# Performance work log

Measured on AMD Instinct MI355X. Metric: run time of the kernel, lower is better.

## Reference

```python
import jax, jax.numpy as jnp
import numpy as np

T, D, K = 8192, 1024, 1024
LMBDA = 5.0
BIG = jnp.float32(3.0e38)  # finite stand-in for +inf so (f - lmbda) stays finite


def setup_inputs() -> dict:
    key = jax.random.key(0)
    k1, k2 = jax.random.split(key)
    return {
        "features": jax.random.normal(k1, (T, D), dtype=jnp.float32),
        "codebook": jax.random.normal(k2, (K, D), dtype=jnp.float32),
    }


def _dpdp(features, codebook, lmbda):
    # squared euclidean distances, (T, K)
    d2 = (
        jnp.sum(features * features, axis=1, keepdims=True)
        - 2.0 * features @ codebook.T
        + jnp.sum(codebook * codebook, axis=1)
    )
    Tn = features.shape[0]
    Kn = codebook.shape[0]

    # Incremental O(T*K) form of the original O(T^2*K) recurrence:
    # f_t[k] = min_{s<=t-1} alpha[s] - lmbda*(t-1-s) + sum_{i=s..t-1} d2[i,k]
    #        = d2[t-1,k] + min(alpha[t-1], f_{t-1}[k] - lmbda)
    # alpha[t] = min_k f_t[k]; beta[t] = start index s of argmin; gamma[t] = argmin_k.
    def fwd_step(carry, inp):
        f, s, alpha = carry  # f:(K,), s:(K,) segment start per codeword, alpha: scalar
        d_t, t = inp
        ext = f - lmbda                      # extend existing segment
        take_new = alpha < ext               # start a new segment at t
        f_new = d_t + jnp.minimum(alpha, ext)
        s_new = jnp.where(take_new, t, s)
        k_star = jnp.argmin(f_new)
        alpha_new = f_new[k_star]
        return (f_new, s_new, alpha_new), (s_new[k_star], k_star.astype(jnp.int32))

    init = (jnp.full((Kn,), BIG, jnp.float32), jnp.zeros((Kn,), jnp.int32), jnp.float32(0.0))
    ts = jnp.arange(Tn, dtype=jnp.int32)
    _, (betas, gammas) = jax.lax.scan(fwd_step, init, (d2, ts))
    # betas[t-1]/gammas[t-1] correspond to alpha index t in the original code.

    # Backtrack: units[beta[cur]:cur] = gamma[cur]; cur = beta[cur].
    def bwd_step(cur, p):
        g = gammas[cur - 1]
        b = betas[cur - 1]
        cur_new = jnp.where(p == b, p, cur)
        return cur_new, g

    _, units = jax.lax.scan(bwd_step, jnp.int32(Tn), ts, reverse=True)
    return units


def reference(features, codebook):
    units = _dpdp(features, codebook, LMBDA)
    quantized = codebook[units]
    quantized_st = features - jax.lax.stop_gradient(features - quantized)
    return quantized_st, units
```

## Files before the change

### kernel.cpp

```cpp
#include <hip/hip_runtime.h>
#include <hip/hip_bf16.h>
#include <stdint.h>

#define T_N 8192
#define K_N 1024
#define D_N 1024
#define LMBDA 5.0f
#define BIGF 3.0e38f
#define CMAX 16
#define THR 26.0f
#define QNAN 0x7FC00000

__global__ __launch_bounds__(256) void k_norms(const float* __restrict__ F,
                                               const float* __restrict__ C,
                                               float* __restrict__ sf2,
                                               float* __restrict__ sc2) {
#pragma clang fp contract(off)
  int wave = threadIdx.x >> 6;
  int lane = threadIdx.x & 63;
  int row = blockIdx.x * 4 + wave;
  const float* src;
  float* dst;
  if (row < T_N) { src = F + (size_t)row * D_N; dst = sf2 + row; }
  else           { src = C + (size_t)(row - T_N) * D_N; dst = sc2 + (row - T_N); }
  int leaf = lane >> 3, j = lane & 7;
  const float* p = src + leaf * 128 + j;
  float x = p[0];
  float r = x * x;
#pragma unroll
  for (int i = 1; i < 16; ++i) {
    float y = p[8 * i];
    r = r + y * y;
  }
  r = r + __shfl_xor(r, 1, 64);
  r = r + __shfl_xor(r, 2, 64);
  r = r + __shfl_xor(r, 4, 64);
  r = r + __shfl_xor(r, 8, 64);
  r = r + __shfl_xor(r, 16, 64);
  r = r + __shfl_xor(r, 32, 64);
  if (lane == 0) *dst = r;
}

__global__ __launch_bounds__(256) void k_gemm(const float* __restrict__ F,
                                              const float* __restrict__ C,
                                              const float* __restrict__ sf2,
                                              const float* __restrict__ sc2,
                                              float* __restrict__ d2) {
  __shared__ float As[32][68];
  __shared__ float Bs[32][132];
  int t0 = (int)(blockIdx.x >> 3) * 64;
  int k0 = (int)(blockIdx.x & 7) * 128;
  int tid = threadIdx.x;
  int tx = tid & 15, ty = tid >> 4;
  float dot[4][8], acc[4][8];
#pragma unroll
  for (int i = 0; i < 4; ++i)
#pragma unroll
    for (int j = 0; j < 8; ++j) { dot[i][j] = 0.0f; acc[i][j] = 0.0f; }
  int ra = tid & 63, ca = (tid >> 6) * 8;
  int rb = tid & 127, cb = (tid >> 7) * 16;
  for (int d0 = 0; d0 < D_N; d0 += 32) {
    __syncthreads();
    {
      const float* fa = &F[(size_t)(t0 + ra) * D_N + d0 + ca];
      float4 a0 = *(const float4*)fa;
      float4 a1 = *(const float4*)(fa + 4);
      As[ca + 0][ra] = a0.x; As[ca + 1][ra] = a0.y; As[ca + 2][ra] = a0.z; As[ca + 3][ra] = a0.w;
      As[ca + 4][ra] = a1.x; As[ca + 5][ra] = a1.y; As[ca + 6][ra] = a1.z; As[ca + 7][ra] = a1.w;
      const float* fb = &C[(size_t)(k0 + rb) * D_N + d0 + cb];
      float4 b0 = *(const float4*)fb;
      float4 b1 = *(const float4*)(fb + 4);
      float4 b2 = *(const float4*)(fb + 8);
      float4 b3 = *(const float4*)(fb + 12);
      Bs[cb + 0][rb] = b0.x; Bs[cb + 1][rb] = b0.y; Bs[cb + 2][rb] = b0.z; Bs[cb + 3][rb] = b0.w;
      Bs[cb + 4][rb] = b1.x; Bs[cb + 5][rb] = b1.y; Bs[cb + 6][rb] = b1.z; Bs[cb + 7][rb] = b1.w;
      Bs[cb + 8][rb] = b2.x; Bs[cb + 9][rb] = b2.y; Bs[cb + 10][rb] = b2.z; Bs[cb + 11][rb] = b2.w;
      Bs[cb + 12][rb] = b3.x; Bs[cb + 13][rb] = b3.y; Bs[cb + 14][rb] = b3.z; Bs[cb + 15][rb] = b3.w;
    }
    __syncthreads();
#pragma unroll
    for (int d = 0; d < 32; ++d) {
      float4 a = *(const float4*)&As[d][ty * 4];
      float4 b0 = *(const float4*)&Bs[d][tx * 4];
      float4 b1 = *(const float4*)&Bs[d][64 + tx * 4];
      float av[4] = {a.x, a.y, a.z, a.w};
      float bv[8] = {b0.x, b0.y, b0.z, b0.w, b1.x, b1.y, b1.z, b1.w};
#pragma unroll
      for (int i = 0; i < 4; ++i)
#pragma unroll
        for (int j = 0; j < 8; ++j)
          acc[i][j] = fmaf(av[i], bv[j], acc[i][j]);
    }
    if (d0 == 352) {
#pragma unroll
      for (int i = 0; i < 4; ++i)
#pragma unroll
        for (int j = 0; j < 8; ++j) { dot[i][j] = acc[i][j]; acc[i][j] = 0.0f; }
    }
    if (d0 == 736) {
#pragma unroll
      for (int i = 0; i < 4; ++i)
#pragma unroll
        for (int j = 0; j < 8; ++j) { dot[i][j] = dot[i][j] + acc[i][j]; acc[i][j] = 0.0f; }
    }
  }
  {
#pragma clang fp contract(off)
#pragma unroll
    for (int i = 0; i < 4; ++i) {
      int t = t0 + ty * 4 + i;
      float sa = sf2[t];
      float o[8];
#pragma unroll
      for (int j = 0; j < 4; ++j) {
        float dsum = dot[i][j] + acc[i][j];
        float two = 2.0f * dsum;
        o[j] = (sa - two) + sc2[k0 + tx * 4 + j];
      }
#pragma unroll
      for (int j = 4; j < 8; ++j) {
        float dsum = dot[i][j] + acc[i][j];
        float two = 2.0f * dsum;
        o[j] = (sa - two) + sc2[k0 + 64 + tx * 4 + (j - 4)];
      }
      float4 o0; o0.x = o[0]; o0.y = o[1]; o0.z = o[2]; o0.w = o[3];
      float4 o1; o1.x = o[4]; o1.y = o[5]; o1.z = o[6]; o1.w = o[7];
      float* dp = &d2[(size_t)t * K_N + k0 + tx * 4];
      *(float4*)dp = o0;
      *(float4*)(dp + 64) = o1;
    }
  }
}

__global__ __launch_bounds__(256) void k_cand(const float* __restrict__ d2,
                                              int2* __restrict__ cand,
                                              float* __restrict__ dminOut) {
  int wave = threadIdx.x >> 6;
  int lane = threadIdx.x & 63;
  int row = blockIdx.x * 4 + wave;
  const float4* p = (const float4*)(d2 + (size_t)row * K_N + lane * 16);
  float4 v0 = p[0], v1 = p[1], v2 = p[2], v3 = p[3];
  float m = fminf(fminf(fminf(v0.x, v0.y), fminf(v0.z, v0.w)),
                  fminf(fminf(v1.x, v1.y), fminf(v1.z, v1.w)));
  float n = fminf(fminf(fminf(v2.x, v2.y), fminf(v2.z, v2.w)),
                  fminf(fminf(v3.x, v3.y), fminf(v3.z, v3.w)));
  m = fminf(m, n);
  m = fminf(m, __shfl_xor(m, 1, 64));
  m = fminf(m, __shfl_xor(m, 2, 64));
  m = fminf(m, __shfl_xor(m, 4, 64));
  m = fminf(m, __shfl_xor(m, 8, 64));
  m = fminf(m, __shfl_xor(m, 16, 64));
  m = fminf(m, __shfl_xor(m, 32, 64));
  if (lane == 0) dminOut[row] = m;
  float thr = m + THR;
  unsigned flags = 0;
#define TESTC(J, VAL) if ((VAL) <= thr) flags |= (1u << (J));
  TESTC(0, v0.x) TESTC(1, v0.y) TESTC(2, v0.z) TESTC(3, v0.w)
  TESTC(4, v1.x) TESTC(5, v1.y) TESTC(6, v1.z) TESTC(7, v1.w)
  TESTC(8, v2.x) TESTC(9, v2.y) TESTC(10, v2.z) TESTC(11, v2.w)
  TESTC(12, v3.x) TESTC(13, v3.y) TESTC(14, v3.z) TESTC(15, v3.w)
#undef TESTC
  int c = __popc(flags);
  int pre = c;
#pragma unroll
  for (int off = 1; off <= 32; off <<= 1) {
    int t = __shfl_up(pre, off, 64);
    if (lane >= off) pre += t;
  }
  int idx = pre - c;
  int2* rowp = cand + (size_t)row * CMAX;
  int kb = lane * 16;
#define EMITC(J, VAL)                                                        \
  if (flags & (1u << (J))) {                                                 \
    if (idx < CMAX) rowp[idx] = make_int2(kb + (J), __float_as_int(VAL));    \
    ++idx;                                                                   \
  }
  EMITC(0, v0.x) EMITC(1, v0.y) EMITC(2, v0.z) EMITC(3, v0.w)
  EMITC(4, v1.x) EMITC(5, v1.y) EMITC(6, v1.z) EMITC(7, v1.w)
  EMITC(8, v2.x) EMITC(9, v2.y) EMITC(10, v2.z) EMITC(11, v2.w)
  EMITC(12, v3.x) EMITC(13, v3.y) EMITC(14, v3.z) EMITC(15, v3.w)
#undef EMITC
}

__global__ __launch_bounds__(256) void k_prev4(const int2* __restrict__ cand,
                                               int4* __restrict__ pb1,
                                               int2* __restrict__ pb2) {
  __shared__ int2 rows[4][5][16];
  int w = threadIdx.x >> 6, lane = threadIdx.x & 63;
  int g = blockIdx.x * 4 + w;
  int base = 4 * g - 1;
  for (int i = lane; i < 80; i += 64) {
    int rr = i >> 4, ss = i & 15;
    int trow = base + rr;
    rows[w][rr][ss] = (trow >= 0) ? cand[(size_t)trow * CMAX + ss] : make_int2(-2, 0);
  }
  __syncthreads();
  int q = 3 - (lane >> 4);
  int s = lane & 15;
  int2 me = rows[w][1 + q][s];
  int k = me.x;
  int pp = -4, p3s = QNAN;
  int d0s = QNAN, d1s = QNAN, d2s = QNAN;
#pragma unroll
  for (int i = 0; i < 16; ++i) {
    if (rows[w][0][i].x == k) { pp = i * 4; p3s = rows[w][0][i].y; }
    if (rows[w][1][i].x == k) d0s = rows[w][1][i].y;
    if (rows[w][2][i].x == k) d1s = rows[w][2][i].y;
    if (rows[w][3][i].x == k) d2s = rows[w][3][i].y;
  }
  if (k < 0) pp = -4;
  pb1[(size_t)g * 64 + lane] = make_int4(pp, me.y, d0s, d1s);
  pb2[(size_t)g * 64 + lane] = make_int2(d2s, p3s);
}

__device__ __forceinline__ float dpp_min16(float x) {
  int t;
  t = __builtin_amdgcn_update_dpp(__float_as_int(x), __float_as_int(x), 0x111, 0xF, 0xF, false);
  x = fminf(x, __int_as_float(t));
  t = __builtin_amdgcn_update_dpp(__float_as_int(x), __float_as_int(x), 0x112, 0xF, 0xF, false);
  x = fminf(x, __int_as_float(t));
  t = __builtin_amdgcn_update_dpp(__float_as_int(x), __float_as_int(x), 0x114, 0xF, 0xF, false);
  x = fminf(x, __int_as_float(t));
  t = __builtin_amdgcn_update_dpp(__float_as_int(x), __float_as_int(x), 0x118, 0xF, 0xF, false);
  x = fminf(x, __int_as_float(t));
  return x;
}
__device__ __forceinline__ float rdlane(float x, int l) {
  return __int_as_float(__builtin_amdgcn_readlane(__float_as_int(x), l));
}

__global__ __launch_bounds__(64, 1) void k_pass1(const int4* __restrict__ pb1,
                                                 const int2* __restrict__ pb2,
                                                 const float* __restrict__ dminArr,
                                                 float* __restrict__ alphaOut) {
  const int lane = threadIdx.x;
  const int q = 3 - (lane >> 4);
  const int4* b1p = pb1 + lane;
  const int2* b2p = pb2 + lane;
  int4 r1[4];
  int2 r2[4];
#pragma unroll
  for (int u = 0; u < 4; ++u) {
    r1[u] = b1p[(size_t)u * 64];
    r2[u] = b2p[(size_t)u * 64];
  }
  float pay = 0.0f;
  float red2c = BIGF;
  float dm2c = 0.0f, dm3c = 0.0f, a1c = 0.0f;
  float areg = 0.0f;
  const int NG = T_N / 4;
  float dmv = dminArr[lane];
  float dmv_next;
  for (int gb = 0; gb < NG; gb += 16) {
    int nb = gb + 16; if (nb >= NG) nb = 0;
    dmv_next = dminArr[nb * 4 + lane];
    for (int g4 = 0; g4 < 16; g4 += 4) {
#pragma unroll
      for (int u = 0; u < 4; ++u) {
        int g = gb + g4 + u;
        int4 pa = r1[u];
        int2 pb = r2[u];
        int g1 = __builtin_amdgcn_ds_bpermute(pa.x, __float_as_int(pay));
        int gn = g + 4; if (gn > NG - 1) gn = NG - 1;
        r1[u] = b1p[(size_t)gn * 64];
        r2[u] = b2p[(size_t)gn * 64];
        float at2p = fminf(rdlane(red2c, 31), dm2c + a1c);
        float ain = fminf(rdlane(red2c, 15), dm3c + at2p);
        int posB = 4 * g - 1;
        if (posB >= 0) {
          areg = (((posB - 1) & 63) == lane) ? at2p : areg;
          areg = ((posB & 63) == lane) ? ain : areg;
          if ((posB & 63) == 63) alphaOut[(posB & ~63) + lane] = areg;
        }
        int r0 = 4 * (g4 + u);
        float dm0 = rdlane(dmv, r0);
        float dm1 = rdlane(dmv, r0 + 1);
        float dm2 = rdlane(dmv, r0 + 2);
        float dm3 = rdlane(dmv, r0 + 3);
        float injE = __int_as_float(pb.y) + at2p;
        float fp = (pa.x < 0) ? BIGF : fminf(__int_as_float(g1), injE);
        float dOwn = __int_as_float(pa.y);
        float d0s = __int_as_float(pa.z);
        float d1s = __int_as_float(pa.w);
        float d2s = __int_as_float(pb.x);
        float A0 = d0s + (fp - LMBDA);
        float A1 = d1s + (A0 - LMBDA);
        float A2 = d2s + (A1 - LMBDA);
        float A3 = dOwn + (A2 - LMBDA);
        float B0 = d0s + ain;
        float B1 = d1s + (B0 - LMBDA);
        float B2 = d2s + (B1 - LMBDA);
        float B3 = dOwn + (B2 - LMBDA);
        float xA = (q == 0) ? A0 : (q == 1) ? A1 : (q == 2) ? A2 : A3;
        float xB = (q == 0) ? B0 : (q == 1) ? B1 : (q == 2) ? B2 : B3;
        float xAB = fminf(xA, xB);
        float red1 = dpp_min16(xAB);
        float a0 = rdlane(red1, 63);
        float a1 = fminf(rdlane(red1, 47), dm1 + a0);
        areg = (((4 * g) & 63) == lane) ? a0 : areg;
        areg = (((4 * g + 1) & 63) == lane) ? a1 : areg;
        float cw1 = d1s + a0;
        float cw2 = d2s + (cw1 - LMBDA);
        float Cin = (q == 2) ? cw1 : cw2;
        float Cterm = dOwn + (Cin - LMBDA);
        float Dterm = dOwn + ((d2s + a1) - LMBDA);
        Dterm = (q == 3) ? Dterm : __int_as_float(QNAN);
        float xr = fminf(fminf(xAB, Cterm), Dterm);
        float red2 = dpp_min16(xr);
        pay = xr;
        red2c = red2;
        dm2c = dm2; dm3c = dm3; a1c = a1;
      }
    }
    dmv = dmv_next;
  }
  float at2 = fminf(rdlane(red2c, 31), dm2c + a1c);
  float at3 = fminf(rdlane(red2c, 15), dm3c + at2);
  areg = ((8190 & 63) == lane) ? at2 : areg;
  areg = ((8191 & 63) == lane) ? at3 : areg;
  alphaOut[(T_N - 64) + lane] = areg;
}

#define CH 128
#define WARM 64
__global__ __launch_bounds__(256) void k_pass2(const float* __restrict__ d2,
                                               const float* __restrict__ AOUT,
                                               unsigned* __restrict__ pack) {
  int kb = blockIdx.x & 3;
  int tc = blockIdx.x >> 2;
  int k = kb * 256 + threadIdx.x;
  int ts = tc * CH;
  int start = ts - WARM; if (start < 0) start = 0;
  int end = ts + CH;
  __shared__ float lal[CH + WARM + 1];
  for (int i = threadIdx.x; i < end - start + 1; i += 256) {
    int idx = start - 1 + i;
    lal[i] = (idx < 0) ? 0.0f : AOUT[idx];
  }
  __syncthreads();
  float f = BIGF;
  unsigned s = 0;
#pragma unroll 4
  for (int tau = start; tau < end; ++tau) {
    float a_in = lal[tau - start];
    float d = d2[(size_t)tau * K_N + k];
    float ext = f - LMBDA;
    if (a_in < ext) s = (unsigned)tau;
    f = d + fminf(a_in, ext);
    if (tau >= ts) {
      float a_out = lal[tau - start + 1];
      if (f == a_out) atomicMin(&pack[tau], ((unsigned)k << 13) | s);
    }
  }
}

__global__ __launch_bounds__(256) void k_backtrack(const unsigned* __restrict__ pack,
                                                   unsigned* __restrict__ unitsWs,
                                                   float* __restrict__ outUnits) {
  __shared__ unsigned lp[T_N];
  __shared__ unsigned long long msk[T_N / 64];
  int tid = threadIdx.x;
  for (int i = tid * 4; i < T_N; i += 1024) {
    *(uint4*)&lp[i] = *(const uint4*)&pack[i];
  }
  __syncthreads();
  if (tid < 64) {
    int lane = tid;
    int cur = T_N;
    for (int B = T_N - 64; B >= 0; B -= 64) {
      unsigned long long marks = 0ull;
      if (cur > B) {
        unsigned pk = lp[B + lane];
        int bv = (int)(pk & 8191u);
        unsigned long long run = __ballot(bv == B + lane);
        while (cur > B) {
          int L = cur - 1 - B;
          unsigned long long below = (L == 63) ? ~0ull : ((1ull << (L + 1)) - 1ull);
          unsigned long long nz = (~run) & below;
          if (nz == 0ull) { marks |= below; cur = B; break; }
          int j = 63 - __builtin_clzll(nz);
          marks |= below & ~((1ull << j) - 1ull);
          int nb = __builtin_amdgcn_readlane(bv, j);
          cur = nb;
          if (cur > B + j) cur = B + j;
        }
      }
      if (lane == 0) msk[B >> 6] = marks;
    }
  }
  __syncthreads();
  for (int p = tid; p < T_N; p += 256) {
    int w = p >> 6;
    unsigned long long m = msk[w] & (~0ull << (p & 63));
    while (m == 0ull) { ++w; m = msk[w]; }
    int idx = (w << 6) + (int)__builtin_ctzll(m);
    unsigned g = (lp[idx] >> 13) & 1023u;
    unitsWs[p] = g;
    outUnits[p] = (float)g;
  }
}

__global__ __launch_bounds__(256) void k_gather(const float* __restrict__ C,
                                                const unsigned* __restrict__ unitsWs,
                                                float* __restrict__ out) {
  int t = blockIdx.x;
  unsigned u = unitsWs[t] & 1023u;
  const float4* src = (const float4*)(C + (size_t)u * D_N);
  float4* dst = (float4*)(out + (size_t)t * D_N);
  dst[threadIdx.x] = src[threadIdx.x];
}

extern "C" void kernel_launch(void* const* d_in, const int* in_sizes, int n_in,
                              void* d_out, int out_size, void* d_ws, size_t ws_size,
                              hipStream_t stream) {
  const float* F = (const float*)d_in[0];
  const float* C = (const float*)d_in[1];
  float* out = (float*)d_out;
  float* d2 = out;
  float* outUnits = out + (size_t)T_N * D_N;
  char* ws = (char*)d_ws;
  float* alphaOut = (float*)(ws);
  unsigned* pack = (unsigned*)(ws + (32 << 10));
  unsigned* unitsWs = (unsigned*)(ws + (64 << 10));
  float* sf2 = (float*)(ws + (96 << 10));
  float* sc2 = (float*)(ws + (128 << 10));
  float* dminArr = (float*)(ws + (160 << 10));
  int2* cand = (int2*)(ws + (1 << 20));
  int4* pb1 = (int4*)(ws + (3 << 20));
  int2* pb2 = (int2*)(ws + (5 << 20));

  k_norms<<<(T_N + K_N) / 4, 256, 0, stream>>>(F, C, sf2, sc2);
  hipMemsetAsync(pack, 0xFF, T_N * sizeof(unsigned), stream);
  hipMemsetAsync(cand, 0xFF, (size_t)T_N * CMAX * sizeof(int2), stream);
  k_gemm<<<(T_N / 64) * (K_N / 128), 256, 0, stream>>>(F, C, sf2, sc2, d2);
  k_cand<<<T_N / 4, 256, 0, stream>>>(d2, cand, dminArr);
  k_prev4<<<(T_N / 4) / 4, 256, 0, stream>>>(cand, pb1, pb2);
  k_pass1<<<1, 64, 0, stream>>>(pb1, pb2, dminArr, alphaOut);
  k_pass2<<<(T_N / CH) * 4, 256, 0, stream>>>(d2, alphaOut, pack);
  k_backtrack<<<1, 256, 0, stream>>>(pack, unitsWs, outUnits);
  k_gather<<<T_N, 256, 0, stream>>>(C, unitsWs, out);
}
```

Baseline: 849.9 us.

## Move Cterm/Dterm injection off the serial pay path via precomputed predecessor distances

k_prev4 now loads two more earlier rows and gives each candidate the distances at the three preceding timesteps, packed into an int4 pb2. k_pass1 rebuilds the previous group's C/D contributions from the carried a0/a1 and these distances. This lets the bpermute payload be set to xAB straight after the first reduction, instead of waiting for the Cterm/Dterm combine and the second reduction. The aim is a shorter serial dependency chain per group in the single-wave recurrence, paid for with extra per-group arithmetic and wider pb2 loads.

```diff
diff --git a/kernel.cpp b/kernel.cpp
--- a/kernel.cpp
+++ b/kernel.cpp
@@ -184,12 +184,12 @@
 
 __global__ __launch_bounds__(256) void k_prev4(const int2* __restrict__ cand,
                                                int4* __restrict__ pb1,
-                                               int2* __restrict__ pb2) {
-  __shared__ int2 rows[4][5][16];
+                                               int4* __restrict__ pb2) {
+  __shared__ int2 rows[4][7][16];
   int w = threadIdx.x >> 6, lane = threadIdx.x & 63;
   int g = blockIdx.x * 4 + w;
-  int base = 4 * g - 1;
-  for (int i = lane; i < 80; i += 64) {
+  int base = 4 * g - 3;
+  for (int i = lane; i < 112; i += 64) {
     int rr = i >> 4, ss = i & 15;
     int trow = base + rr;
     rows[w][rr][ss] = (trow >= 0) ? cand[(size_t)trow * CMAX + ss] : make_int2(-2, 0);
@@ -197,20 +197,23 @@
   __syncthreads();
   int q = 3 - (lane >> 4);
   int s = lane & 15;
-  int2 me = rows[w][1 + q][s];
+  int2 me = rows[w][3 + q][s];
   int k = me.x;
-  int pp = -4, p3s = QNAN;
+  int pp = -4;
+  int pe1 = QNAN, pe2 = QNAN, pe3 = QNAN;
   int d0s = QNAN, d1s = QNAN, d2s = QNAN;
 #pragma unroll
   for (int i = 0; i < 16; ++i) {
-    if (rows[w][0][i].x == k) { pp = i * 4; p3s = rows[w][0][i].y; }
-    if (rows[w][1][i].x == k) d0s = rows[w][1][i].y;
-    if (rows[w][2][i].x == k) d1s = rows[w][2][i].y;
-    if (rows[w][3][i].x == k) d2s = rows[w][3][i].y;
+    if (rows[w][0][i].x == k) pe1 = rows[w][0][i].y;
+    if (rows[w][1][i].x == k) pe2 = rows[w][1][i].y;
+    if (rows[w][2][i].x == k) { pp = i * 4; pe3 = rows[w][2][i].y; }
+    if (rows[w][3][i].x == k) d0s = rows[w][3][i].y;
+    if (rows[w][4][i].x == k) d1s = rows[w][4][i].y;
+    if (rows[w][5][i].x == k) d2s = rows[w][5][i].y;
   }
   if (k < 0) pp = -4;
   pb1[(size_t)g * 64 + lane] = make_int4(pp, me.y, d0s, d1s);
-  pb2[(size_t)g * 64 + lane] = make_int2(d2s, p3s);
+  pb2[(size_t)g * 64 + lane] = make_int4(d2s, pe3, pe1, pe2);
 }
 
 __device__ __forceinline__ float dpp_min16(float x) {
@@ -230,15 +233,14 @@
 }
 
 __global__ __launch_bounds__(64, 1) void k_pass1(const int4* __restrict__ pb1,
-                                                 const int2* __restrict__ pb2,
+                                                 const int4* __restrict__ pb2,
                                                  const float* __restrict__ dminArr,
                                                  float* __restrict__ alphaOut) {
   const int lane = threadIdx.x;
   const int q = 3 - (lane >> 4);
   const int4* b1p = pb1 + lane;
-  const int2* b2p = pb2 + lane;
-  int4 r1[4];
-  int2 r2[4];
+  const int4* b2p = pb2 + lane;
+  int4 r1[4], r2[4];
 #pragma unroll
   for (int u = 0; u < 4; ++u) {
     r1[u] = b1p[(size_t)u * 64];
@@ -246,7 +248,7 @@
   }
   float pay = 0.0f;
   float red2c = BIGF;
-  float dm2c = 0.0f, dm3c = 0.0f, a1c = 0.0f;
+  float dm2c = 0.0f, dm3c = 0.0f, a1c = 0.0f, a0c = 0.0f;
   float areg = 0.0f;
   const int NG = T_N / 4;
   float dmv = dminArr[lane];
@@ -259,7 +261,7 @@
       for (int u = 0; u < 4; ++u) {
         int g = gb + g4 + u;
         int4 pa = r1[u];
-        int2 pb = r2[u];
+        int4 pb = r2[u];
         int g1 = __builtin_amdgcn_ds_bpermute(pa.x, __float_as_int(pay));
         int gn = g + 4; if (gn > NG - 1) gn = NG - 1;
         r1[u] = b1p[(size_t)gn * 64];
@@ -277,8 +279,17 @@
         float dm1 = rdlane(dmv, r0 + 1);
         float dm2 = rdlane(dmv, r0 + 2);
         float dm3 = rdlane(dmv, r0 + 3);
-        float injE = __int_as_float(pb.y) + at2p;
-        float fp = (pa.x < 0) ? BIGF : fminf(__int_as_float(g1), injE);
+        float pe1 = __int_as_float(pb.z);
+        float pe2 = __int_as_float(pb.w);
+        float pe3 = __int_as_float(pb.y);
+        float Cw1 = pe1 + a0c;
+        float Cw2 = pe2 + (Cw1 - LMBDA);
+        float c3r = pe3 + (Cw2 - LMBDA);
+        float Dw2 = pe2 + a1c;
+        float d3r = pe3 + (Dw2 - LMBDA);
+        float injE = pe3 + at2p;
+        float inj = fminf(fminf(c3r, d3r), injE);
+        float fp = (pa.x < 0) ? BIGF : fminf(__int_as_float(g1), inj);
         float dOwn = __int_as_float(pa.y);
         float d0s = __int_as_float(pa.z);
         float d1s = __int_as_float(pa.w);
@@ -294,6 +305,7 @@
         float xA = (q == 0) ? A0 : (q == 1) ? A1 : (q == 2) ? A2 : A3;
         float xB = (q == 0) ? B0 : (q == 1) ? B1 : (q == 2) ? B2 : B3;
         float xAB = fminf(xA, xB);
+        pay = xAB;
         float red1 = dpp_min16(xAB);
         float a0 = rdlane(red1, 63);
         float a1 = fminf(rdlane(red1, 47), dm1 + a0);
@@ -306,10 +318,8 @@
         float Dterm = dOwn + ((d2s + a1) - LMBDA);
         Dterm = (q == 3) ? Dterm : __int_as_float(QNAN);
         float xr = fminf(fminf(xAB, Cterm), Dterm);
-        float red2 = dpp_min16(xr);
-        pay = xr;
-        red2c = red2;
-        dm2c = dm2; dm3c = dm3; a1c = a1;
+        red2c = dpp_min16(xr);
+        dm2c = dm2; dm3c = dm3; a1c = a1; a0c = a0;
       }
     }
     dmv = dmv_next;
@@ -427,7 +437,7 @@
   float* dminArr = (float*)(ws + (160 << 10));
   int2* cand = (int2*)(ws + (1 << 20));
   int4* pb1 = (int4*)(ws + (3 << 20));
-  int2* pb2 = (int2*)(ws + (5 << 20));
+  int4* pb2 = (int4*)(ws + (5 << 20));
 
   k_norms<<<(T_N + K_N) / 4, 256, 0, stream>>>(F, C, sf2, sc2);
   hipMemsetAsync(pack, 0xFF, T_N * sizeof(unsigned), stream);
```

Result: slower. 875.8 us (+3.0%).
